# Optimization experiments

Hardware: AMD Instinct MI355X
Metric: run time of the kernel (lower is better)

Reference implementation:

```python
import jax, jax.numpy as jnp
import numpy as np

B, C, H, W = 4, 256, 56, 56
N = H * W  # 3136 tokens


def setup_inputs() -> dict:
    key = jax.random.key(0)
    ks = jax.random.split(key, 12)
    f = lambda k, s: jax.random.normal(k, s, dtype=jnp.float32)
    return {
        "feat0": f(ks[0], (B, 1, C, H, W)),
        "feat1": f(ks[1], (B, 1, C, H, W)),
        "feat2": f(ks[2], (B, 1, C, H, W)),
        "feat3": f(ks[3], (B, 1, C, H, W)),
        "hist0": jax.random.uniform(ks[4], (B, N), dtype=jnp.float32),
        "hist1": jax.random.uniform(ks[5], (B, N), dtype=jnp.float32),
        "hist2": jax.random.uniform(ks[6], (B, N), dtype=jnp.float32),
        "mask": f(ks[7], (N, N)),
        "Wv": f(ks[8], (C, C)) * 0.02,   # v_linear weight (torch layout [out,in])
        "bv": jnp.zeros((C,), jnp.float32),
        "Wl": f(ks[9], (C, 2 * C)) * 0.02,  # low_channel weight
        "bl": jnp.zeros((C,), jnp.float32),
    }


def _tokens(x5d):
    # [b,1,c,h,w] -> [b, n, c]
    b = x5d.shape[0]
    return x5d.reshape(b, C, N).transpose(0, 2, 1)


def _to5d(tok):
    # [b,n,c] -> [b,1,c,h,w]
    b = tok.shape[0]
    return tok.transpose(0, 2, 1).reshape(b, 1, C, H, W)


def reference(feat0, feat1, feat2, feat3, hist0, hist1, hist2, mask, Wv, bv, Wl, bl):
    scale = 1.0 / jnp.sqrt(jnp.float32(C))

    def stage(q_tok, feat5d):
        f = _tokens(feat5d)                                   # [b,n,c]
        corr = jnp.einsum('bnc,bmc->bnm', q_tok, f) * scale   # [b,n,n]
        p = jax.nn.softmax(corr + mask[None], axis=-1)        # masked softmax
        v = f @ Wv.T + bv                                     # v_linear
        motion = jnp.einsum('bnm,bmc->bnc', p, v)             # attention
        refined = motion + f                                  # residual
        out = jnp.concatenate([refined, f], axis=-1) @ Wl.T + bl  # low_channel
        return refined, out

    # histograms (hist0..hist2) are consumed by the original module but its
    # histogram_mask is dead code; they do not affect the math.
    q = _tokens(feat0)
    refined, out1 = stage(q, feat1)
    refined, out2 = stage(refined, feat2)
    refined, out3 = stage(refined, feat3)

    return jnp.concatenate(
        [feat0, _to5d(out1), _to5d(out2), _to5d(out3)], axis=1
    )  # [b, 4, c, h, w]
```

## Files before the change

kernel.cpp:

```cpp
#include <hip/hip_runtime.h>
#include <hip/hip_bf16.h>

#define B_   4
#define C_   256
#define N_   3136
#define QT_  196
#define NKV_ 98
#define CH_  5

typedef __attribute__((ext_vector_type(8)))  short bf16x8;
typedef __attribute__((ext_vector_type(4)))  float f32x4;
typedef __attribute__((ext_vector_type(16))) float f32x16;

#define LOG2E  1.4426950408889634f
#define SCALE2 (LOG2E / 16.0f)
#define FMAX_  20.0f

__device__ __forceinline__ unsigned short bfbits(float f) {
  __hip_bfloat16 h = __float2bfloat16(f);
  return *(unsigned short*)&h;
}
__device__ __forceinline__ unsigned cvtpk(float lo, float hi) {
  unsigned r;
  asm("v_cvt_pk_bf16_f32 %0, %1, %2" : "=v"(r) : "v"(lo), "v"(hi));
  return r;
}

__device__ __forceinline__ void gld16(const void* g, void* l) {
  __builtin_amdgcn_global_load_lds(
      (const __attribute__((address_space(1))) unsigned int*)g,
      (__attribute__((address_space(3))) unsigned int*)l, 16, 0, 0);
}

__device__ __forceinline__ int vperm(int n) {
  int k = n & 31;
  return (n & ~31) | (k & 16) | (((k >> 2) & 1) << 3) | (k & 3) | (((k >> 3) & 1) << 2);
}

__global__ __launch_bounds__(256) void transpose4_kernel(
    const float* __restrict__ f0, const float* __restrict__ f1,
    const float* __restrict__ f2, const float* __restrict__ f3,
    __hip_bfloat16* __restrict__ d0, __hip_bfloat16* __restrict__ d1,
    __hip_bfloat16* __restrict__ d2, __hip_bfloat16* __restrict__ d3,
    float* __restrict__ out) {
  __shared__ float tile[32][33];
  const int z  = blockIdx.z;
  const int fi = z >> 2;
  const int b  = z & 3;
  const float* src = (fi == 0) ? f0 : (fi == 1) ? f1 : (fi == 2) ? f2 : f3;
  __hip_bfloat16* dst = (fi == 0) ? d0 : (fi == 1) ? d1 : (fi == 2) ? d2 : d3;
  const int n0 = blockIdx.x * 32;
  const int c0 = blockIdx.y * 32;
  const int tx = threadIdx.x & 31;
  const int ty = threadIdx.x >> 5;
  const float* s = src + (size_t)b * C_ * N_;
  float* ob = out + (size_t)b * 4 * C_ * N_;
#pragma unroll
  for (int i = 0; i < 4; ++i) {
    int c = c0 + ty + i * 8;
    float v = s[(size_t)c * N_ + n0 + tx];
    tile[ty + i * 8][tx] = v;
    if (fi == 0) ob[(size_t)c * N_ + n0 + tx] = v;
  }
  __syncthreads();
  __hip_bfloat16* d = dst + (size_t)b * N_ * C_;
#pragma unroll
  for (int i = 0; i < 4; ++i) {
    int n = n0 + ty + i * 8;
    d[(size_t)n * C_ + c0 + tx] = __float2bfloat16(tile[tx][ty + i * 8]);
  }
}

__global__ __launch_bounds__(256) void cvt_all_kernel(
    const float* __restrict__ Wv, const float* __restrict__ Wl,
    const float* __restrict__ mask,
    __hip_bfloat16* __restrict__ Wvb, __hip_bfloat16* __restrict__ Wlb,
    __hip_bfloat16* __restrict__ maskb) {
  int i = blockIdx.x * 256 + threadIdx.x;
  if (i < 24576) {
    const float* src; __hip_bfloat16* dst; int off;
    if (i < 8192) { src = Wv; dst = Wvb; off = i; }
    else          { src = Wl; dst = Wlb; off = i - 8192; }
    const float4* s4 = (const float4*)src;
    float4 a = s4[2 * off], b = s4[2 * off + 1];
    union { unsigned short u[8]; bf16x8 v; } p;
    p.u[0]=bfbits(a.x); p.u[1]=bfbits(a.y); p.u[2]=bfbits(a.z); p.u[3]=bfbits(a.w);
    p.u[4]=bfbits(b.x); p.u[5]=bfbits(b.y); p.u[6]=bfbits(b.z); p.u[7]=bfbits(b.w);
    *(bf16x8*)(dst + 8 * off) = p.v;
    return;
  }
  int j = i - 24576;
  if (j >= NKV_ * NKV_ * 32 * 2) return;
  const int hi  = j & 1;
  const int cl  = (j >> 1) & 31;
  const int rem = j >> 6;
  const int kt  = rem % NKV_;
  const int qu  = rem / NKV_;
  const int q   = qu * 32 + cl;
  const float* s = mask + (size_t)q * N_ + kt * 32 + 4 * hi;
  float4 a0 = *(const float4*)(s);
  float4 a1 = *(const float4*)(s + 8);
  float4 a2 = *(const float4*)(s + 16);
  float4 a3 = *(const float4*)(s + 24);
  union { unsigned short u[16]; bf16x8 v[2]; } p;
  p.u[0]=bfbits(a0.x*LOG2E); p.u[1]=bfbits(a0.y*LOG2E); p.u[2]=bfbits(a0.z*LOG2E); p.u[3]=bfbits(a0.w*LOG2E);
  p.u[4]=bfbits(a1.x*LOG2E); p.u[5]=bfbits(a1.y*LOG2E); p.u[6]=bfbits(a1.z*LOG2E); p.u[7]=bfbits(a1.w*LOG2E);
  p.u[8]=bfbits(a2.x*LOG2E); p.u[9]=bfbits(a2.y*LOG2E); p.u[10]=bfbits(a2.z*LOG2E); p.u[11]=bfbits(a2.w*LOG2E);
  p.u[12]=bfbits(a3.x*LOG2E); p.u[13]=bfbits(a3.y*LOG2E); p.u[14]=bfbits(a3.z*LOG2E); p.u[15]=bfbits(a3.w*LOG2E);
  __hip_bfloat16* d = maskb + ((size_t)rem * 32 + cl) * 32 + hi * 16;
  *(bf16x8*)(d)     = p.v[0];
  *(bf16x8*)(d + 8) = p.v[1];
}

__global__ __launch_bounds__(256) void v_linear_kernel(
    const __hip_bfloat16* __restrict__ f1, const __hip_bfloat16* __restrict__ f2,
    const __hip_bfloat16* __restrict__ f3,
    const __hip_bfloat16* __restrict__ Wv, const float* __restrict__ bv,
    __hip_bfloat16* __restrict__ vT0, __hip_bfloat16* __restrict__ vT1,
    __hip_bfloat16* __restrict__ vT2)
{
  const int s    = blockIdx.z;
  const int b    = blockIdx.y;
  const int nblk = blockIdx.x;
  const __hip_bfloat16* fb = (s == 0) ? f1 : (s == 1) ? f2 : f3;
  __hip_bfloat16* vT = (s == 0) ? vT0 : (s == 1) ? vT1 : vT2;
  const int wave = threadIdx.x >> 6;
  const int lane = threadIdx.x & 63;
  const int qt = lane & 15, g = lane >> 4;
  const int n0 = nblk * 64;
  const __hip_bfloat16* fbb = fb + (size_t)b * N_ * C_;
  const int c0 = wave * 64;
  f32x4 acc[4][4];
#pragma unroll
  for (int u = 0; u < 4; ++u)
#pragma unroll
    for (int j = 0; j < 4; ++j) acc[u][j] = (f32x4){0.f, 0.f, 0.f, 0.f};
#pragma unroll
  for (int kk = 0; kk < 8; ++kk) {
    int ko = kk * 32 + g * 8;
    bf16x8 bb[4];
#pragma unroll
    for (int j = 0; j < 4; ++j)
      bb[j] = *(const bf16x8*)(fbb + (size_t)(n0 + j * 16 + qt) * C_ + ko);
#pragma unroll
    for (int u = 0; u < 4; ++u) {
      bf16x8 a = *(const bf16x8*)(Wv + (size_t)(c0 + u * 16 + qt) * C_ + ko);
#pragma unroll
      for (int j = 0; j < 4; ++j)
        acc[u][j] = __builtin_amdgcn_mfma_f32_16x16x32_bf16(a, bb[j], acc[u][j], 0, 0, 0);
    }
  }
  __hip_bfloat16* outp = vT + (size_t)b * C_ * N_;
#pragma unroll
  for (int u = 0; u < 4; ++u)
#pragma unroll
    for (int j = 0; j < 4; ++j)
#pragma unroll
      for (int r = 0; r < 4; ++r) {
        int c = c0 + u * 16 + 4 * g + r;
        int n = vperm(n0 + j * 16 + qt);
        outp[(size_t)c * N_ + n] = __float2bfloat16(acc[u][j][r] + bv[c]);
      }
}

__global__ __launch_bounds__(256, 2) void attn_kernel(
    const __hip_bfloat16* __restrict__ qb,
    const __hip_bfloat16* __restrict__ kb,
    const __hip_bfloat16* __restrict__ vT,
    const __hip_bfloat16* __restrict__ mb,
    unsigned* __restrict__ pOb,
    float* __restrict__ pML)
{
  __shared__ __hip_bfloat16 Kl[2][32 * 256];
  __shared__ __hip_bfloat16 Vl[2][32 * 256];

  const int bid   = blockIdx.x;
  const int grp   = bid % 20;
  const int qblk  = bid / 20;
  const int b     = grp / CH_;
  const int chunk = grp % CH_;
  const int wave  = threadIdx.x >> 6;
  const int lane  = threadIdx.x & 63;
  const int cl = lane & 31, hi = lane >> 5;
  const int qunit = qblk * 4 + wave;
  const bool valid = qunit < 98;
  const int qu = valid ? qunit : 97;
  const int q0row = qu * 32 + cl;
  const int t0 = (chunk * NKV_) / CH_;
  const int t1 = ((chunk + 1) * NKV_) / CH_;
  const int nt = t1 - t0;
  const int tid = threadIdx.x;

  const __hip_bfloat16* qbb = qb + (size_t)b * N_ * C_;
  const char* kbbc = (const char*)(kb + (size_t)b * N_ * C_);
  const char* vbbc = (const char*)(vT + (size_t)b * C_ * N_);
  const char* mbase = (const char*)mb + (size_t)qu * (NKV_ * 2048) + cl * 64 + hi * 32;

  bf16x8 qa[16];
#pragma unroll
  for (int ks = 0; ks < 16; ++ks)
    qa[ks] = *(const bf16x8*)(qbb + (size_t)q0row * C_ + ks * 16 + 8 * hi);

  f32x16 o[8];
#pragma unroll
  for (int ct = 0; ct < 8; ++ct)
#pragma unroll
    for (int r = 0; r < 16; ++r) o[ct][r] = 0.f;
  float lsum = 0.f;

  auto STAGE = [&](int buf, int t) {
    const char* ks0 = kbbc + (size_t)t * 32 * 512;
#pragma unroll
    for (int i = 0; i < 4; ++i) {
      int g2 = tid + i * 256;
      int ks = g2 >> 6, h2 = (g2 >> 5) & 1, key = g2 & 31;
      gld16(ks0 + key * 512 + ks * 32 + h2 * 16, (char*)&Kl[buf][0] + g2 * 16);
    }
    const char* vs0 = vbbc + (size_t)t * 64;
#pragma unroll
    for (int i = 0; i < 4; ++i) {
      int g2 = tid + i * 256;
      int st = g2 >> 9, h2 = (g2 >> 8) & 1, c = g2 & 255;
      gld16(vs0 + (size_t)c * (N_ * 2) + st * 32 + h2 * 16, (char*)&Vl[buf][0] + g2 * 16);
    }
  };

  union { uint4 v[2]; unsigned w[8]; } mm;
  auto MLOAD = [&](int t) {
    mm.v[0] = *(const uint4*)(mbase + (size_t)t * 2048);
    mm.v[1] = *(const uint4*)(mbase + (size_t)t * 2048 + 16);
  };

  STAGE(0, t0);
  MLOAD(t0);

  const int kread = hi * 512 + cl * 16;
  const int vread = hi * 4096 + cl * 16;

  for (int tt = 0; tt < nt; ++tt) {
    const int buf = tt & 1;
    const bool nl = (tt + 1 < nt);
    if (nl) STAGE(buf ^ 1, t0 + tt + 1);
    if (nl) asm volatile("s_waitcnt vmcnt(10)" ::: "memory");
    else    asm volatile("s_waitcnt vmcnt(2)"  ::: "memory");
    __builtin_amdgcn_s_barrier();

    f32x16 s;
#pragma unroll
    for (int r = 0; r < 16; ++r) s[r] = 0.f;
    if (valid) {
      const char* Kb = (const char*)&Kl[buf][0] + kread;
      __builtin_amdgcn_s_setprio(1);
#pragma unroll
      for (int ks = 0; ks < 16; ++ks) {
        bf16x8 kf = *(const bf16x8*)(Kb + ks * 1024);
        s = __builtin_amdgcn_mfma_f32_32x32x16_bf16(kf, qa[ks], s, 0, 0, 0);
      }
      __builtin_amdgcn_s_setprio(0);
    }
    if (nl) asm volatile("s_waitcnt vmcnt(8)" ::: "memory");
    else    asm volatile("s_waitcnt vmcnt(0)" ::: "memory");

    if (valid) {
      float p[16];
#pragma unroll
      for (int j = 0; j < 16; ++j) {
        unsigned wo = mm.w[j >> 1];
        float mf = __uint_as_float((j & 1) ? (wo & 0xffff0000u) : (wo << 16));
        p[j] = exp2f(fmaf(s[j], SCALE2, mf) - FMAX_);
      }
      lsum += ((p[0]+p[1])+(p[2]+p[3])) + ((p[4]+p[5])+(p[6]+p[7]))
            + ((p[8]+p[9])+(p[10]+p[11])) + ((p[12]+p[13])+(p[14]+p[15]));

      union { unsigned u[4]; bf16x8 v8; } A0, A1;
#pragma unroll
      for (int k = 0; k < 4; ++k) A0.u[k] = cvtpk(p[2 * k], p[2 * k + 1]);
#pragma unroll
      for (int k = 0; k < 4; ++k) A1.u[k] = cvtpk(p[8 + 2 * k], p[9 + 2 * k]);

      const char* Vb = (const char*)&Vl[buf][0] + vread;
      __builtin_amdgcn_s_setprio(1);
#pragma unroll
      for (int ct = 0; ct < 8; ++ct) {
        bf16x8 vf0 = *(const bf16x8*)(Vb + ct * 512);
        o[ct] = __builtin_amdgcn_mfma_f32_32x32x16_bf16(A0.v8, vf0, o[ct], 0, 0, 0);
        bf16x8 vf1 = *(const bf16x8*)(Vb + 8192 + ct * 512);
        o[ct] = __builtin_amdgcn_mfma_f32_32x32x16_bf16(A1.v8, vf1, o[ct], 0, 0, 0);
      }
      __builtin_amdgcn_s_setprio(0);
    }
    if (nl) MLOAD(t0 + tt + 1);
    __builtin_amdgcn_s_barrier();
  }

  if (valid) {
    float lt = lsum + __shfl_xor(lsum, 32);
#pragma unroll
    for (int r = 0; r < 16; ++r) {
      int q = (r & 3) + 8 * (r >> 2) + 4 * hi;
      int qt16 = qu * 2 + (q >> 4);
      int row = q & 15;
      size_t ob = ((((size_t)b * QT_ + qt16) * CH_ + chunk) * 2048) + row * 128 + cl;
#pragma unroll
      for (int pp = 0; pp < 4; ++pp)
        pOb[ob + pp * 32] = cvtpk(o[2 * pp][r], o[2 * pp + 1][r]);
    }
    if (lane < 32) {
      int qt16 = qu * 2 + (cl >> 4);
      int row = cl & 15;
      float* pml = pML + (((size_t)b * QT_ + qt16) * CH_ + chunk) * 32;
      pml[row] = FMAX_;
      pml[16 + row] = lt;
    }
  }
}

__global__ __launch_bounds__(256) void combine_kernel(
    const unsigned* __restrict__ pOb, const float* __restrict__ pML,
    const __hip_bfloat16* __restrict__ fb,
    __hip_bfloat16* __restrict__ ref)
{
  __shared__ float sml[CH_ * 32];
  const int b = blockIdx.y;
  const int qtile = blockIdx.x;
  const int tid = threadIdx.x;
  const float* pml = pML + ((size_t)b * QT_ + qtile) * (CH_ * 32);
  if (tid < CH_ * 32) sml[tid] = pml[tid];
  __syncthreads();

  const int w  = tid & 127;
  const int r0 = (tid >> 7) * 8;
  const int ch_lo = 64 * (w >> 5) + (w & 31);
  const int ch_hi = ch_lo + 32;

  float wgt[CH_][8];
#pragma unroll
  for (int r = 0; r < 8; ++r) {
    int row = r0 + r;
    float M = sml[row];
#pragma unroll
    for (int ch = 1; ch < CH_; ++ch) M = fmaxf(M, sml[ch * 32 + row]);
    float L = 0.f;
#pragma unroll
    for (int ch = 0; ch < CH_; ++ch) {
      float wv = exp2f(sml[ch * 32 + row] - M);
      wgt[ch][r] = wv;
      L += wv * sml[ch * 32 + 16 + row];
    }
    float iL = 1.f / L;
#pragma unroll
    for (int ch = 0; ch < CH_; ++ch) wgt[ch][r] *= iL;
  }

  float acc_lo[8], acc_hi[8];
#pragma unroll
  for (int r = 0; r < 8; ++r) { acc_lo[r] = 0.f; acc_hi[r] = 0.f; }
  const unsigned* base = pOb + ((size_t)b * QT_ + qtile) * (CH_ * 2048) + r0 * 128 + w;
#pragma unroll
  for (int ch = 0; ch < CH_; ++ch) {
    const unsigned* p = base + ch * 2048;
#pragma unroll
    for (int r = 0; r < 8; ++r) {
      unsigned u = p[r * 128];
      acc_lo[r] += wgt[ch][r] * __uint_as_float(u << 16);
      acc_hi[r] += wgt[ch][r] * __uint_as_float(u & 0xffff0000u);
    }
  }

  const __hip_bfloat16* f = fb + ((size_t)b * N_ + qtile * 16 + r0) * C_;
  __hip_bfloat16* rf = ref + ((size_t)b * N_ + qtile * 16 + r0) * C_;
#pragma unroll
  for (int r = 0; r < 8; ++r) {
    rf[r * C_ + ch_lo] = __float2bfloat16(acc_lo[r] + __bfloat162float(f[r * C_ + ch_lo]));
    rf[r * C_ + ch_hi] = __float2bfloat16(acc_hi[r] + __bfloat162float(f[r * C_ + ch_hi]));
  }
}

__global__ __launch_bounds__(256) void out_linear_kernel(
    const __hip_bfloat16* __restrict__ refb,
    const __hip_bfloat16* __restrict__ fb,
    const __hip_bfloat16* __restrict__ Wl,
    const float* __restrict__ bl,
    float* __restrict__ out)
{
  const int b    = blockIdx.z;
  const int cblk = blockIdx.y;
  const int nblk = blockIdx.x;
  const int wave = threadIdx.x >> 6;
  const int lane = threadIdx.x & 63;
  const int qt = lane & 15, g = lane >> 4;
  const int c0 = cblk * 64 + wave * 16;
  const int n0 = nblk * 64;
  const __hip_bfloat16* rb  = refb + (size_t)b * N_ * C_;
  const __hip_bfloat16* fbb = fb  + (size_t)b * N_ * C_;
  f32x4 acc[4];
#pragma unroll
  for (int j = 0; j < 4; ++j) acc[j] = (f32x4){0.f, 0.f, 0.f, 0.f};
#pragma unroll
  for (int kk = 0; kk < 8; ++kk) {
    int ko = kk * 32 + g * 8;
    bf16x8 a = *(const bf16x8*)(Wl + (size_t)(c0 + qt) * 512 + ko);
#pragma unroll
    for (int j = 0; j < 4; ++j) {
      bf16x8 bb = *(const bf16x8*)(rb + (size_t)(n0 + j * 16 + qt) * C_ + ko);
      acc[j] = __builtin_amdgcn_mfma_f32_16x16x32_bf16(a, bb, acc[j], 0, 0, 0);
    }
  }
#pragma unroll
  for (int kk = 0; kk < 8; ++kk) {
    int ko = kk * 32 + g * 8;
    bf16x8 a = *(const bf16x8*)(Wl + (size_t)(c0 + qt) * 512 + 256 + ko);
#pragma unroll
    for (int j = 0; j < 4; ++j) {
      bf16x8 bb = *(const bf16x8*)(fbb + (size_t)(n0 + j * 16 + qt) * C_ + ko);
      acc[j] = __builtin_amdgcn_mfma_f32_16x16x32_bf16(a, bb, acc[j], 0, 0, 0);
    }
  }
  float* ob = out + (size_t)b * 4 * C_ * N_;
#pragma unroll
  for (int j = 0; j < 4; ++j)
#pragma unroll
    for (int r = 0; r < 4; ++r) {
      int c = c0 + 4 * g + r;
      int n = n0 + j * 16 + qt;
      ob[(size_t)c * N_ + n] = acc[j][r] + bl[c];
    }
}

extern "C" void kernel_launch(void* const* d_in, const int* in_sizes, int n_in,
                              void* d_out, int out_size, void* d_ws, size_t ws_size,
                              hipStream_t stream) {
  (void)in_sizes; (void)n_in; (void)out_size; (void)ws_size;
  const float* feat0 = (const float*)d_in[0];
  const float* feat1 = (const float*)d_in[1];
  const float* feat2 = (const float*)d_in[2];
  const float* feat3 = (const float*)d_in[3];
  const float* mask  = (const float*)d_in[7];
  const float* Wv    = (const float*)d_in[8];
  const float* bv    = (const float*)d_in[9];
  const float* Wl    = (const float*)d_in[10];
  const float* bl    = (const float*)d_in[11];
  float* out = (float*)d_out;

  const size_t TOKB = (size_t)B_ * N_ * C_ * 2;
  char* w = (char*)d_ws;
  __hip_bfloat16* q0   = (__hip_bfloat16*)(w);
  __hip_bfloat16* f1   = (__hip_bfloat16*)(w + TOKB);
  __hip_bfloat16* f2   = (__hip_bfloat16*)(w + 2 * TOKB);
  __hip_bfloat16* f3   = (__hip_bfloat16*)(w + 3 * TOKB);
  __hip_bfloat16* vT0  = (__hip_bfloat16*)(w + 4 * TOKB);
  __hip_bfloat16* vT1  = (__hip_bfloat16*)(w + 5 * TOKB);
  __hip_bfloat16* vT2  = (__hip_bfloat16*)(w + 6 * TOKB);
  char* w2 = w + 7 * TOKB;
  __hip_bfloat16* Wv_bf = (__hip_bfloat16*)(w2);
  __hip_bfloat16* Wl_bf = (__hip_bfloat16*)(w2 + 131072);
  __hip_bfloat16* maskb = (__hip_bfloat16*)(w2 + 393216);
  unsigned* pOb         = (unsigned*)(w2 + 393216 + 19668992);
  float* pML            = (float*)(w2 + 393216 + 19668992 + (size_t)B_ * QT_ * CH_ * 4096 * 2);

  dim3 tb(256);
  transpose4_kernel<<<dim3(98, 8, 16), tb, 0, stream>>>(feat0, feat1, feat2, feat3,
                                                        q0, f1, f2, f3, out);
  cvt_all_kernel<<<dim3((24576 + NKV_ * NKV_ * 64 + 255) / 256), tb, 0, stream>>>(
      Wv, Wl, mask, Wv_bf, Wl_bf, maskb);
  v_linear_kernel<<<dim3(49, 4, 3), tb, 0, stream>>>(f1, f2, f3, Wv_bf, bv,
                                                     vT0, vT1, vT2);

  const __hip_bfloat16* fs[3] = {f1, f2, f3};
  const __hip_bfloat16* vTs[3] = {vT0, vT1, vT2};
  __hip_bfloat16* refs[3] = {vT0, vT1, vT0};
  const __hip_bfloat16* q = q0;
  for (int s = 0; s < 3; ++s) {
    attn_kernel<<<dim3(500), tb, 0, stream>>>(q, fs[s], vTs[s], maskb, pOb, pML);
    combine_kernel<<<dim3(196, 4), tb, 0, stream>>>(pOb, pML, fs[s], refs[s]);
    out_linear_kernel<<<dim3(49, 4, 4), tb, 0, stream>>>(refs[s], fs[s], Wl_bf, bl,
                                                         out + (size_t)(s + 1) * C_ * N_);
    q = refs[s];
  }
}
```

Before: 379.1 us.

## Split QK MFMA chain into two accumulators and retile output linear kernel

In the attention kernel, the serial chain of 16 dependent MFMAs for the score tile is split into two independent accumulator chains that are summed before the exponent. This is meant to hide MFMA dependency latency. The explicit vmcnt wait before the softmax step is removed, so ordering of the mask load now relies on the compiler's own waitcnt insertion. The output linear kernel is retiled so each wave covers 32 channels by 32 tokens over a merged K loop of 16 steps, reusing each token fragment across two weight fragments, and the grid changes to match.

```diff
diff --git a/kernel.cpp b/kernel.cpp
--- a/kernel.cpp
+++ b/kernel.cpp
@@ -245,21 +245,21 @@
     else    asm volatile("s_waitcnt vmcnt(2)"  ::: "memory");
     __builtin_amdgcn_s_barrier();
 
-    f32x16 s;
-#pragma unroll
-    for (int r = 0; r < 16; ++r) s[r] = 0.f;
+    f32x16 sA, sB;
+#pragma unroll
+    for (int r = 0; r < 16; ++r) { sA[r] = 0.f; sB[r] = 0.f; }
     if (valid) {
       const char* Kb = (const char*)&Kl[buf][0] + kread;
       __builtin_amdgcn_s_setprio(1);
 #pragma unroll
-      for (int ks = 0; ks < 16; ++ks) {
-        bf16x8 kf = *(const bf16x8*)(Kb + ks * 1024);
-        s = __builtin_amdgcn_mfma_f32_32x32x16_bf16(kf, qa[ks], s, 0, 0, 0);
+      for (int ks = 0; ks < 8; ++ks) {
+        bf16x8 kf0 = *(const bf16x8*)(Kb + ks * 2048);
+        bf16x8 kf1 = *(const bf16x8*)(Kb + ks * 2048 + 1024);
+        sA = __builtin_amdgcn_mfma_f32_32x32x16_bf16(kf0, qa[2 * ks],     sA, 0, 0, 0);
+        sB = __builtin_amdgcn_mfma_f32_32x32x16_bf16(kf1, qa[2 * ks + 1], sB, 0, 0, 0);
       }
       __builtin_amdgcn_s_setprio(0);
     }
-    if (nl) asm volatile("s_waitcnt vmcnt(8)" ::: "memory");
-    else    asm volatile("s_waitcnt vmcnt(0)" ::: "memory");
 
     if (valid) {
       float p[16];
@@ -267,7 +267,7 @@
       for (int j = 0; j < 16; ++j) {
         unsigned wo = mm.w[j >> 1];
         float mf = __uint_as_float((j & 1) ? (wo & 0xffff0000u) : (wo << 16));
-        p[j] = exp2f(fmaf(s[j], SCALE2, mf) - FMAX_);
+        p[j] = exp2f(fmaf(sA[j] + sB[j], SCALE2, mf) - FMAX_);
       }
       lsum += ((p[0]+p[1])+(p[2]+p[3])) + ((p[4]+p[5])+(p[6]+p[7]))
             + ((p[8]+p[9])+(p[10]+p[11])) + ((p[12]+p[13])+(p[14]+p[15]));
@@ -389,42 +389,40 @@
   const int wave = threadIdx.x >> 6;
   const int lane = threadIdx.x & 63;
   const int qt = lane & 15, g = lane >> 4;
-  const int c0 = cblk * 64 + wave * 16;
-  const int n0 = nblk * 64;
+  const int c0 = cblk * 128 + wave * 32;
+  const int n0 = nblk * 32;
   const __hip_bfloat16* rb  = refb + (size_t)b * N_ * C_;
   const __hip_bfloat16* fbb = fb  + (size_t)b * N_ * C_;
-  f32x4 acc[4];
-#pragma unroll
-  for (int j = 0; j < 4; ++j) acc[j] = (f32x4){0.f, 0.f, 0.f, 0.f};
-#pragma unroll
-  for (int kk = 0; kk < 8; ++kk) {
+  f32x4 acc[2][2];
+#pragma unroll
+  for (int u = 0; u < 2; ++u)
+#pragma unroll
+    for (int j = 0; j < 2; ++j) acc[u][j] = (f32x4){0.f, 0.f, 0.f, 0.f};
+#pragma unroll
+  for (int kk = 0; kk < 16; ++kk) {
     int ko = kk * 32 + g * 8;
-    bf16x8 a = *(const bf16x8*)(Wl + (size_t)(c0 + qt) * 512 + ko);
-#pragma unroll
-    for (int j = 0; j < 4; ++j) {
-      bf16x8 bb = *(const bf16x8*)(rb + (size_t)(n0 + j * 16 + qt) * C_ + ko);
-      acc[j] = __builtin_amdgcn_mfma_f32_16x16x32_bf16(a, bb, acc[j], 0, 0, 0);
-    }
-  }
-#pragma unroll
-  for (int kk = 0; kk < 8; ++kk) {
-    int ko = kk * 32 + g * 8;
-    bf16x8 a = *(const bf16x8*)(Wl + (size_t)(c0 + qt) * 512 + 256 + ko);
-#pragma unroll
-    for (int j = 0; j < 4; ++j) {
-      bf16x8 bb = *(const bf16x8*)(fbb + (size_t)(n0 + j * 16 + qt) * C_ + ko);
-      acc[j] = __builtin_amdgcn_mfma_f32_16x16x32_bf16(a, bb, acc[j], 0, 0, 0);
+    const __hip_bfloat16* src = (kk < 8) ? rb : fbb;
+    int ko2 = ko & 255;
+    bf16x8 bb0 = *(const bf16x8*)(src + (size_t)(n0 + qt) * C_ + ko2);
+    bf16x8 bb1 = *(const bf16x8*)(src + (size_t)(n0 + 16 + qt) * C_ + ko2);
+#pragma unroll
+    for (int u = 0; u < 2; ++u) {
+      bf16x8 a = *(const bf16x8*)(Wl + (size_t)(c0 + u * 16 + qt) * 512 + ko);
+      acc[u][0] = __builtin_amdgcn_mfma_f32_16x16x32_bf16(a, bb0, acc[u][0], 0, 0, 0);
+      acc[u][1] = __builtin_amdgcn_mfma_f32_16x16x32_bf16(a, bb1, acc[u][1], 0, 0, 0);
     }
   }
   float* ob = out + (size_t)b * 4 * C_ * N_;
 #pragma unroll
-  for (int j = 0; j < 4; ++j)
-#pragma unroll
-    for (int r = 0; r < 4; ++r) {
-      int c = c0 + 4 * g + r;
-      int n = n0 + j * 16 + qt;
-      ob[(size_t)c * N_ + n] = acc[j][r] + bl[c];
-    }
+  for (int u = 0; u < 2; ++u)
+#pragma unroll
+    for (int j = 0; j < 2; ++j)
+#pragma unroll
+      for (int r = 0; r < 4; ++r) {
+        int c = c0 + u * 16 + 4 * g + r;
+        int n = n0 + j * 16 + qt;
+        ob[(size_t)c * N_ + n] = acc[u][j][r] + bl[c];
+      }
 }
 
 extern "C" void kernel_launch(void* const* d_in, const int* in_sizes, int n_in,
@@ -473,7 +471,7 @@
   for (int s = 0; s < 3; ++s) {
     attn_kernel<<<dim3(500), tb, 0, stream>>>(q, fs[s], vTs[s], maskb, pOb, pML);
     combine_kernel<<<dim3(196, 4), tb, 0, stream>>>(pOb, pML, fs[s], refs[s]);
-    out_linear_kernel<<<dim3(49, 4, 4), tb, 0, stream>>>(refs[s], fs[s], Wl_bf, bl,
+    out_linear_kernel<<<dim3(98, 2, 4), tb, 0, stream>>>(refs[s], fs[s], Wl_bf, bl,
                                                          out + (size_t)(s + 1) * C_ * N_);
     q = refs[s];
   }
```

Result: no change. 383.8 us (+1.2%).
